# Kernel tuning notes

Hardware: AMD Instinct MI355X
Metric: run time of the kernel (lower is better)

## Reference

```python
import jax, jax.numpy as jnp
import numpy as np

B, S, E = 2, 2048, 1024
H = 16
D = E // H  # head dim

def setup_inputs() -> dict:
    key = jax.random.key(0)
    ks = jax.random.split(key, 9)
    s = 1.0 / np.sqrt(E)
    return {
        "hidden_states": jax.random.normal(ks[0], (B, S, E), dtype=jnp.float32),
        "Wq": jax.random.normal(ks[1], (E, E), dtype=jnp.float32) * s,
        "bq": jnp.zeros((E,), jnp.float32),
        "Wk": jax.random.normal(ks[2], (E, E), dtype=jnp.float32) * s,
        "bk": jnp.zeros((E,), jnp.float32),
        "Wv": jax.random.normal(ks[3], (E, E), dtype=jnp.float32) * s,
        "bv": jnp.zeros((E,), jnp.float32),
        "Wo": jax.random.normal(ks[4], (E, E), dtype=jnp.float32) * s,
        "bo": jnp.zeros((E,), jnp.float32),
    }

def _split_heads(x):
    # [B,S,E] -> [B,H,S,D]
    b, s, _ = x.shape
    return x.reshape(b, s, H, D).transpose(0, 2, 1, 3)

def reference(hidden_states, Wq, bq, Wk, bk, Wv, bv, Wo, bo):
    q = _split_heads(hidden_states @ Wq + bq)  # [B,H,S,D]
    k = _split_heads(hidden_states @ Wk + bk)
    v = _split_heads(hidden_states @ Wv + bv)
    scores = jnp.einsum('bhqd,bhkd->bhqk', q, k) / jnp.sqrt(jnp.float32(D))
    probs = jax.nn.softmax(scores, axis=-1)  # [B,H,S,S]
    ctx = jnp.einsum('bhqk,bhkd->bhqd', probs, v)
    ctx = ctx.transpose(0, 2, 1, 3).reshape(hidden_states.shape[0], -1, E)
    out = ctx @ Wo + bo
    return out, probs
```

## Files before the change

### kernel.cpp

```cpp
#include <hip/hip_runtime.h>
#include <hip/hip_bf16.h>
#include <stdint.h>


typedef __attribute__((ext_vector_type(8))) short bf16x8;
typedef __attribute__((ext_vector_type(4))) short bf16x4v;
typedef __attribute__((ext_vector_type(4))) float f32x4;

#define DEV static __device__ __forceinline__

DEV short f2bs(float f) {
  union { __hip_bfloat16 b; short s; } u;
  u.b = __float2bfloat16(f);
  return u.s;
}
DEV f32x4 mfma16(bf16x8 a, bf16x8 b, f32x4 c) {
  return __builtin_amdgcn_mfma_f32_16x16x32_bf16(a, b, c, 0, 0, 0);
}
DEV float fexp2(float x) { return __builtin_amdgcn_exp2f(x); }
typedef const __attribute__((address_space(1))) void* gas1_t;
typedef __attribute__((address_space(3))) void* las3_t;
DEV void gload_lds16(const void* g, void* l) {
  __builtin_amdgcn_global_load_lds((gas1_t)(uintptr_t)g, (las3_t)(uint32_t)(uintptr_t)l,
                                   16, 0, 0);
}
#define WAIT_VMCNT(N) asm volatile("s_waitcnt vmcnt(" #N ")" ::: "memory")
#define WAIT_LGKM0() asm volatile("s_waitcnt lgkmcnt(0)" ::: "memory")
#define BARRIER() do { __builtin_amdgcn_s_barrier(); __builtin_amdgcn_sched_barrier(0); } while (0)

__global__ void cvt_all_kernel(const float* __restrict__ X,
                               const float* __restrict__ Wq, const float* __restrict__ Wk,
                               const float* __restrict__ Wv, const float* __restrict__ Wo,
                               short* __restrict__ Xb, short* __restrict__ Wt) {
  __shared__ short tile[64][68];
  int bx = blockIdx.x, t = threadIdx.x;
  if (bx < 2048) {
    size_t i = (size_t)bx * 256 + t;
    const float4* X4 = (const float4*)X;
    float4 a = X4[2 * i], c = X4[2 * i + 1];
    bf16x8 o;
    o[0] = f2bs(a.x); o[1] = f2bs(a.y); o[2] = f2bs(a.z); o[3] = f2bs(a.w);
    o[4] = f2bs(c.x); o[5] = f2bs(c.y); o[6] = f2bs(c.z); o[7] = f2bs(c.w);
    *(bf16x8*)(Xb + i * 8) = o;
    return;
  }
  int wb = bx - 2048;
  int mat = wb >> 8, rem = wb & 255;
  const float* W = mat == 0 ? Wq : mat == 1 ? Wk : mat == 2 ? Wv : Wo;
  int kb = (rem >> 4) * 64, nb = (rem & 15) * 64;
#pragma unroll
  for (int it = 0; it < 4; ++it) {
    int idx = it * 256 + t;
    int row = idx >> 4, c4 = (idx & 15) * 4;
    float4 v = *(const float4*)(W + (size_t)(kb + row) * 1024 + nb + c4);
    tile[row][c4 + 0] = f2bs(v.x); tile[row][c4 + 1] = f2bs(v.y);
    tile[row][c4 + 2] = f2bs(v.z); tile[row][c4 + 3] = f2bs(v.w);
  }
  __syncthreads();
#pragma unroll
  for (int it = 0; it < 4; ++it) {
    int idx = it * 256 + t;
    int rn = idx >> 4, c4 = (idx & 15) * 4;
    bf16x4v o;
    o[0] = tile[c4 + 0][rn]; o[1] = tile[c4 + 1][rn];
    o[2] = tile[c4 + 2][rn]; o[3] = tile[c4 + 3][rn];
    *(bf16x4v*)(Wt + (((size_t)mat) << 20) + (size_t)(nb + rn) * 1024 + kb + c4) = o;
  }
}

template <int MODE, int GBX>
__global__ __launch_bounds__(256, 2)
void gemm_bt_kernel(const short* __restrict__ A, const short* __restrict__ Bt,
                    const float* __restrict__ bias0, const float* __restrict__ bias1,
                    const float* __restrict__ bias2,
                    short* __restrict__ o0, short* __restrict__ o1, short* __restrict__ o2,
                    float* __restrict__ fout) {
  __shared__ short As[2][128 * 32];
  __shared__ short Bs[2][128 * 32];
  const int nwg = GBX * gridDim.y;
  const int cpx = nwg >> 3;
  const int bid0 = blockIdx.y * GBX + blockIdx.x;
  const int bid = (bid0 % 8) * cpx + bid0 / 8;
  const int m0 = (bid % GBX) * 128, n0 = (bid / GBX) * 128;
  const int t = threadIdx.x, w = t >> 6, l = t & 63, g = l >> 4, r = l & 15;
  const int wr = (w >> 1) * 64, wc = (w & 1) * 64;
  f32x4 acc[4][4] = {};

#define STAGE_G(k0_, b_)                                                                   \
  do {                                                                                     \
    gload_lds16(A + (size_t)(m0 + (t >> 2)) * 1024 + (k0_) + (t & 3) * 8, As[b_] + w * 512); \
    gload_lds16(A + (size_t)(m0 + 64 + (t >> 2)) * 1024 + (k0_) + (t & 3) * 8,             \
                As[b_] + 2048 + w * 512);                                                  \
    gload_lds16(Bt + (size_t)(n0 + (t >> 2)) * 1024 + (k0_) + (t & 3) * 8, Bs[b_] + w * 512); \
    gload_lds16(Bt + (size_t)(n0 + 64 + (t >> 2)) * 1024 + (k0_) + (t & 3) * 8,            \
                Bs[b_] + 2048 + w * 512);                                                  \
  } while (0)

  STAGE_G(0, 0);
  for (int it = 0; it < 32; ++it) {
    const int cur = it & 1;
    if (it < 31) {
      STAGE_G((it + 1) * 32, cur ^ 1);
      WAIT_VMCNT(4);
    } else {
      WAIT_VMCNT(0);
    }
    BARRIER();
    bf16x8 af[4], bfv[4];
#pragma unroll
    for (int i = 0; i < 4; i++) af[i] = *(const bf16x8*)(As[cur] + (wr + i * 16 + r) * 32 + g * 8);
#pragma unroll
    for (int j = 0; j < 4; j++) bfv[j] = *(const bf16x8*)(Bs[cur] + (wc + j * 16 + r) * 32 + g * 8);
    __builtin_amdgcn_s_setprio(1);
#pragma unroll
    for (int i = 0; i < 4; i++)
#pragma unroll
      for (int j = 0; j < 4; j++) acc[i][j] = mfma16(af[i], bfv[j], acc[i][j]);
    __builtin_amdgcn_s_setprio(0);
    BARRIER();
  }
#undef STAGE_G
  if constexpr (MODE == 0) {
#pragma unroll
    for (int j = 0; j < 4; j++) {
      int ng = n0 + wc + j * 16 + r;
      int mat = ng >> 10, nn = ng & 1023, hh = nn >> 6, dd = nn & 63;
      const float* bp = mat == 0 ? bias0 : (mat == 1 ? bias1 : bias2);
      short* dst = mat == 0 ? o0 : (mat == 1 ? o1 : o2);
      float bv = bp[nn];
      float sc = (mat == 0) ? 0.18033688f : 1.0f;
#pragma unroll
      for (int i = 0; i < 4; i++) {
#pragma unroll
        for (int q = 0; q < 4; q++) {
          int m = m0 + wr + i * 16 + g * 4 + q;
          int bb = m >> 11, ss = m & 2047;
          dst[((size_t)(bb * 16 + hh) * 2048 + ss) * 64 + dd] = f2bs((acc[i][j][q] + bv) * sc);
        }
      }
    }
  } else {
#pragma unroll
    for (int i = 0; i < 4; i++)
#pragma unroll
      for (int q = 0; q < 4; q++) {
        int m = m0 + wr + i * 16 + g * 4 + q;
#pragma unroll
        for (int j = 0; j < 4; j++) {
          int ng = n0 + wc + j * 16 + r;
          fout[(size_t)m * 1024 + ng] = acc[i][j][q] + bias0[ng];
        }
      }
  }
}

__global__ __launch_bounds__(256, 2)
void attn_kernel(const short* __restrict__ Qm, const short* __restrict__ Km,
                 const short* __restrict__ Vm, float* __restrict__ probs,
                 short* __restrict__ ctx) {
  __shared__ short Ks[2][128 * 64];
  __shared__ short Vt[64 * 136];
  __shared__ short Ps[4][16 * 136];
  __shared__ float rls[128];
  const int f = blockIdx.x;
  const int wgid = (f & 7) * 64 + (f >> 3);
  const int bh = wgid >> 4, q0 = (wgid & 15) * 128;
  const int bb = bh >> 4, hh = bh & 15;
  const short* Qp = Qm + (size_t)bh * 2048 * 64;
  const short* Kp = Km + (size_t)bh * 2048 * 64;
  const short* Vp = Vm + (size_t)bh * 2048 * 64;
  float* Pp = probs + (size_t)bh * 2048 * 2048;
  const int t = threadIdx.x, w = t >> 6, l = t & 63, g = l >> 4, r = l & 15;
  const int lr = l >> 3, lc = l & 7;
  const int swz = lc ^ lr;

#define STAGE_K(kt_, buf_)                                                            \
  do {                                                                                \
    const short* src_ = Kp + (size_t)((kt_) * 128) * 64;                              \
    _Pragma("unroll") for (int it_ = 0; it_ < 4; ++it_)                               \
        gload_lds16(src_ + (size_t)(it_ * 32 + w * 8 + lr) * 64 + swz * 8,            \
                    Ks[buf_] + (it_ * 32 + w * 8) * 64);                              \
  } while (0)

#pragma unroll
  for (int it = 0; it < 2; ++it) {
    gload_lds16(Qp + (size_t)(q0 + it * 32 + w * 8 + lr) * 64 + swz * 8,
                Ks[0] + (it * 32 + w * 8) * 64);
    gload_lds16(Qp + (size_t)(q0 + 64 + it * 32 + w * 8 + lr) * 64 + swz * 8,
                Ks[1] + (it * 32 + w * 8) * 64);
  }
  __syncthreads();
  bf16x8 qf0[2], qf1[2];
#pragma unroll
  for (int df = 0; df < 2; df++) {
    qf0[df] = *(const bf16x8*)(Ks[0] + (w * 16 + r) * 64 + ((df * 4 + g) ^ (r & 7)) * 8);
    qf1[df] = *(const bf16x8*)(Ks[1] + (w * 16 + r) * 64 + ((df * 4 + g) ^ (r & 7)) * 8);
  }
  WAIT_LGKM0();
  BARRIER();

  float lrow0 = 0.f;
  STAGE_K(0, 0);
  for (int kt = 0; kt < 16; ++kt) {
    const int cur = kt & 1;
    if (kt < 15) {
      STAGE_K(kt + 1, cur ^ 1);
      WAIT_VMCNT(4);
    } else {
      WAIT_VMCNT(0);
    }
    BARRIER();
    f32x4 st[8] = {};
    __builtin_amdgcn_s_setprio(1);
#pragma unroll
    for (int df = 0; df < 2; ++df) {
      bf16x8 kf[8];
#pragma unroll
      for (int ni = 0; ni < 8; ni++)
        kf[ni] = *(const bf16x8*)(Ks[cur] + (ni * 16 + r) * 64 + ((df * 4 + g) ^ (r & 7)) * 8);
#pragma unroll
      for (int ni = 0; ni < 8; ni++) st[ni] = mfma16(kf[ni], qf0[df], st[ni]);
    }
    __builtin_amdgcn_s_setprio(0);
    float ssum = 0.f;
#pragma unroll
    for (int ni = 0; ni < 8; ni++)
#pragma unroll
      for (int q4 = 0; q4 < 4; q4++) ssum += fexp2(st[ni][q4]);
    ssum += __shfl_xor(ssum, 16);
    ssum += __shfl_xor(ssum, 32);
    lrow0 += ssum;
    BARRIER();
  }
  const float rinv0 = 1.0f / lrow0;
  if (g == 0) rls[w * 16 + r] = rinv0;

  const int kp = (t >> 3) * 2, d0v = (t & 7) * 8, lcv = t & 7, kunit = t >> 5;

#define B_TILE_BODY(stv_, qrow_, rinv_)                                                \
  do {                                                                                 \
                              \
    _Pragma("unroll") for (int ni = 0; ni < 8; ni++) {                                 \
      bf16x4v pk;                                                                      \
      _Pragma("unroll") for (int q4 = 0; q4 < 4; q4++) {                               \
        float pe = fexp2((stv_)[ni][q4]);                                              \
        (stv_)[ni][q4] = pe;                                                           \
        pk[q4] = f2bs(pe);                                                             \
      }                                                                                \
      *(bf16x4v*)(&Ps[w][r * 136 + ni * 16 + g * 4]) = pk;                             \
    }                                                                                  \
                               \
    _Pragma("unroll") for (int e = 0; e < 8; e++) {                                    \
      unsigned int p0_ = (unsigned int)(unsigned short)v0[e] |                         \
                         ((unsigned int)(unsigned short)v1[e] << 16);                  \
      unsigned int p1_ = (unsigned int)(unsigned short)v2[e] |                         \
                         ((unsigned int)(unsigned short)v3[e] << 16);                  \
      *(unsigned int*)(Vt + (d0v + e) * 136 + ((kunit ^ lcv) << 3) + (kp & 7)) = p0_;  \
      *(unsigned int*)(Vt + (d0v + e) * 136 + ((8 + (kunit ^ lcv)) << 3) + (kp & 7)) = p1_; \
    }                                                                                  \
    WAIT_LGKM0();                                                                      \
    BARRIER();                                                                         \
              \
    _Pragma("unroll") for (int ni = 0; ni < 8; ni++) {                                 \
      f32x4 pr;                                                                        \
      _Pragma("unroll") for (int q4 = 0; q4 < 4; q4++) pr[q4] = (stv_)[ni][q4] * (rinv_); \
      *(f32x4*)(Pp + (size_t)((qrow_) + w * 16 + r) * 2048 + kt * 128 + ni * 16 + g * 4) = pr; \
    }                                                                                  \
                             \
    __builtin_amdgcn_s_setprio(1);                                                     \
    _Pragma("unroll") for (int kf4 = 0; kf4 < 4; ++kf4) {                              \
      bf16x8 pa, vb[4];                                                                \
      pa = *(const bf16x8*)(&Ps[w][r * 136 + kf4 * 32 + g * 8]);                       \
      _Pragma("unroll") for (int nj = 0; nj < 4; nj++) {                               \
        int u_ = kf4 * 4 + g, x_ = nj * 2 + (r >> 3);                                  \
        int su_ = (u_ & 8) | ((u_ & 7) ^ x_);                                          \
        vb[nj] = *(const bf16x8*)(Vt + (nj * 16 + r) * 136 + (su_ << 3));              \
      }                                                                                \
      _Pragma("unroll") for (int nj = 0; nj < 4; nj++)                                 \
          cacc[nj] = mfma16(pa, vb[nj], cacc[nj]);                                     \
    }                                                                                  \
    __builtin_amdgcn_s_setprio(0);                                                     \
  } while (0)

  f32x4 cacc[4] = {};
  float lrow1 = 0.f;
  STAGE_K(0, 0);
  for (int kt = 0; kt < 16; ++kt) {
    const int cur = kt & 1;
    bf16x8 v0 = *(const bf16x8*)(Vp + (size_t)(kt * 128 + kp) * 64 + d0v);
    bf16x8 v1 = *(const bf16x8*)(Vp + (size_t)(kt * 128 + kp + 1) * 64 + d0v);
    bf16x8 v2 = *(const bf16x8*)(Vp + (size_t)(kt * 128 + 64 + kp) * 64 + d0v);
    bf16x8 v3 = *(const bf16x8*)(Vp + (size_t)(kt * 128 + 64 + kp + 1) * 64 + d0v);
    if (kt < 15) STAGE_K(kt + 1, cur ^ 1);
    if (kt == 0) { WAIT_VMCNT(8); }
    else if (kt < 15) { WAIT_VMCNT(16); }
    else { WAIT_VMCNT(12); }
    BARRIER();
    f32x4 st0[8] = {}, st1[8] = {};
    __builtin_amdgcn_s_setprio(1);
#pragma unroll
    for (int df = 0; df < 2; ++df) {
      bf16x8 kf[8];
#pragma unroll
      for (int ni = 0; ni < 8; ni++)
        kf[ni] = *(const bf16x8*)(Ks[cur] + (ni * 16 + r) * 64 + ((df * 4 + g) ^ (r & 7)) * 8);
#pragma unroll
      for (int ni = 0; ni < 8; ni++) {
        st0[ni] = mfma16(kf[ni], qf0[df], st0[ni]);
        st1[ni] = mfma16(kf[ni], qf1[df], st1[ni]);
      }
    }
    __builtin_amdgcn_s_setprio(0);
    {
      float ssum = 0.f;
#pragma unroll
      for (int ni = 0; ni < 8; ni++)
#pragma unroll
        for (int q4 = 0; q4 < 4; q4++) ssum += fexp2(st1[ni][q4]);
      ssum += __shfl_xor(ssum, 16);
      ssum += __shfl_xor(ssum, 32);
      lrow1 += ssum;
    }
    B_TILE_BODY(st0, q0, rinv0);
  }
#pragma unroll
  for (int nj = 0; nj < 4; nj++)
#pragma unroll
    for (int q4 = 0; q4 < 4; q4++) {
      int qt = w * 16 + g * 4 + q4;
      float val = cacc[nj][q4] * rls[qt];
      ctx[((size_t)(bb * 2048 + q0 + qt)) * 1024 + hh * 64 + nj * 16 + r] = f2bs(val);
    }

  const float rinv1 = 1.0f / lrow1;
  if (g == 0) rls[64 + w * 16 + r] = rinv1;
#pragma unroll
  for (int nj = 0; nj < 4; nj++) cacc[nj] = (f32x4){0.f, 0.f, 0.f, 0.f};
  STAGE_K(0, 0);
  for (int kt = 0; kt < 16; ++kt) {
    const int cur = kt & 1;
    bf16x8 v0 = *(const bf16x8*)(Vp + (size_t)(kt * 128 + kp) * 64 + d0v);
    bf16x8 v1 = *(const bf16x8*)(Vp + (size_t)(kt * 128 + kp + 1) * 64 + d0v);
    bf16x8 v2 = *(const bf16x8*)(Vp + (size_t)(kt * 128 + 64 + kp) * 64 + d0v);
    bf16x8 v3 = *(const bf16x8*)(Vp + (size_t)(kt * 128 + 64 + kp + 1) * 64 + d0v);
    if (kt < 15) STAGE_K(kt + 1, cur ^ 1);
    if (kt == 0) { WAIT_VMCNT(8); }
    else if (kt < 15) { WAIT_VMCNT(16); }
    else { WAIT_VMCNT(12); }
    BARRIER();
    f32x4 st[8] = {};
    __builtin_amdgcn_s_setprio(1);
#pragma unroll
    for (int df = 0; df < 2; ++df) {
      bf16x8 kf[8];
#pragma unroll
      for (int ni = 0; ni < 8; ni++)
        kf[ni] = *(const bf16x8*)(Ks[cur] + (ni * 16 + r) * 64 + ((df * 4 + g) ^ (r & 7)) * 8);
#pragma unroll
      for (int ni = 0; ni < 8; ni++) st[ni] = mfma16(kf[ni], qf1[df], st[ni]);
    }
    __builtin_amdgcn_s_setprio(0);
    B_TILE_BODY(st, q0 + 64, rinv1);
  }
#pragma unroll
  for (int nj = 0; nj < 4; nj++)
#pragma unroll
    for (int q4 = 0; q4 < 4; q4++) {
      int qt = w * 16 + g * 4 + q4;
      float val = cacc[nj][q4] * rls[64 + qt];
      ctx[((size_t)(bb * 2048 + q0 + 64 + qt)) * 1024 + hh * 64 + nj * 16 + r] = f2bs(val);
    }
#undef B_TILE_BODY
#undef STAGE_K
}

extern "C" void kernel_launch(void* const* d_in, const int* in_sizes, int n_in,
                              void* d_out, int out_size, void* d_ws, size_t ws_size,
                              hipStream_t stream) {
  (void)in_sizes; (void)n_in; (void)out_size; (void)ws_size;
  const float* X  = (const float*)d_in[0];
  const float* Wq = (const float*)d_in[1];
  const float* bq = (const float*)d_in[2];
  const float* Wk = (const float*)d_in[3];
  const float* bk = (const float*)d_in[4];
  const float* Wv = (const float*)d_in[5];
  const float* bv = (const float*)d_in[6];
  const float* Wo = (const float*)d_in[7];
  const float* bo = (const float*)d_in[8];
  float* out = (float*)d_out;
  float* probs = out + (size_t)2 * 2048 * 1024;

  short* Xb = (short*)d_ws;
  short* Wt = Xb + (size_t)4194304;
  short* Qb = Wt + (size_t)4194304;
  short* Kb = Qb + (size_t)4194304;
  short* Vb = Kb + (size_t)4194304;
  short* Cx = Vb + (size_t)4194304;

  cvt_all_kernel<<<3072, 256, 0, stream>>>(X, Wq, Wk, Wv, Wo, Xb, Wt);
  gemm_bt_kernel<0, 32><<<dim3(32, 24), 256, 0, stream>>>(Xb, Wt, bq, bk, bv,
                                                          Qb, Kb, Vb, nullptr);
  attn_kernel<<<512, 256, 0, stream>>>(Qb, Kb, Vb, probs, Cx);
  gemm_bt_kernel<1, 32><<<dim3(32, 8), 256, 0, stream>>>(Cx, Wt + (size_t)3 * 1048576, bo,
                                                         nullptr, nullptr, nullptr, nullptr,
                                                         nullptr, out);
}
```

Baseline: 222.6 us.

## Software-pipeline attention tiles so QK MFMA overlaps previous tile's PV and prob stores

Restructures the per-tile attention loop into a two-stage software pipeline with ping-pong score registers. Each iteration computes QK^T for tile kt and then finishes tile kt-1 (normalized prob stores and the PV MFMAs) before exponentiating and staging the current tile's P and V into LDS. This is meant to hide the LDS barrier and exp latency behind MFMA work. In exchange it holds two score buffers live, which raises register pressure, and it needs more intricate vmcnt waits that must stay correct.

```diff
diff --git a/kernel.cpp b/kernel.cpp
--- a/kernel.cpp
+++ b/kernel.cpp
@@ -237,36 +237,19 @@
 
   const int kp = (t >> 3) * 2, d0v = (t & 7) * 8, lcv = t & 7, kunit = t >> 5;
 
-#define B_TILE_BODY(stv_, qrow_, rinv_)                                                \
+#define V_LOADS(kt_)                                                                   \
+  v0 = *(const bf16x8*)(Vp + (size_t)((kt_) * 128 + kp) * 64 + d0v);                   \
+  v1 = *(const bf16x8*)(Vp + (size_t)((kt_) * 128 + kp + 1) * 64 + d0v);               \
+  v2 = *(const bf16x8*)(Vp + (size_t)((kt_) * 128 + 64 + kp) * 64 + d0v);              \
+  v3 = *(const bf16x8*)(Vp + (size_t)((kt_) * 128 + 64 + kp + 1) * 64 + d0v)
+
+#define FIN_T(stP_, qrow_, rinv_, ktF_)                                                \
   do {                                                                                 \
-                              \
-    _Pragma("unroll") for (int ni = 0; ni < 8; ni++) {                                 \
-      bf16x4v pk;                                                                      \
-      _Pragma("unroll") for (int q4 = 0; q4 < 4; q4++) {                               \
-        float pe = fexp2((stv_)[ni][q4]);                                              \
-        (stv_)[ni][q4] = pe;                                                           \
-        pk[q4] = f2bs(pe);                                                             \
-      }                                                                                \
-      *(bf16x4v*)(&Ps[w][r * 136 + ni * 16 + g * 4]) = pk;                             \
-    }                                                                                  \
-                               \
-    _Pragma("unroll") for (int e = 0; e < 8; e++) {                                    \
-      unsigned int p0_ = (unsigned int)(unsigned short)v0[e] |                         \
-                         ((unsigned int)(unsigned short)v1[e] << 16);                  \
-      unsigned int p1_ = (unsigned int)(unsigned short)v2[e] |                         \
-                         ((unsigned int)(unsigned short)v3[e] << 16);                  \
-      *(unsigned int*)(Vt + (d0v + e) * 136 + ((kunit ^ lcv) << 3) + (kp & 7)) = p0_;  \
-      *(unsigned int*)(Vt + (d0v + e) * 136 + ((8 + (kunit ^ lcv)) << 3) + (kp & 7)) = p1_; \
-    }                                                                                  \
-    WAIT_LGKM0();                                                                      \
-    BARRIER();                                                                         \
-              \
     _Pragma("unroll") for (int ni = 0; ni < 8; ni++) {                                 \
       f32x4 pr;                                                                        \
-      _Pragma("unroll") for (int q4 = 0; q4 < 4; q4++) pr[q4] = (stv_)[ni][q4] * (rinv_); \
-      *(f32x4*)(Pp + (size_t)((qrow_) + w * 16 + r) * 2048 + kt * 128 + ni * 16 + g * 4) = pr; \
-    }                                                                                  \
-                             \
+      _Pragma("unroll") for (int q4 = 0; q4 < 4; q4++) pr[q4] = (stP_)[ni][q4] * (rinv_); \
+      *(f32x4*)(Pp + (size_t)((qrow_) + w * 16 + r) * 2048 + (ktF_) * 128 + ni * 16 + g * 4) = pr; \
+    }                                                                                  \
     __builtin_amdgcn_s_setprio(1);                                                     \
     _Pragma("unroll") for (int kf4 = 0; kf4 < 4; ++kf4) {                              \
       bf16x8 pa, vb[4];                                                                \
@@ -282,46 +265,87 @@
     __builtin_amdgcn_s_setprio(0);                                                     \
   } while (0)
 
+#define B_ITER(kt_, stC_, stP_, HAS_FIN, FIRST, SECOND, LAST, T1, qf_, qrow_, rinv_)   \
+  do {                                                                                 \
+    const int cur_ = (kt_) & 1;                                                        \
+    bf16x4v pk[8];                                                                     \
+    V_LOADS(kt_);                                                                      \
+    if (!(LAST)) STAGE_K((kt_) + 1, cur_ ^ 1);                                         \
+    if ((FIRST) || (SECOND)) { WAIT_VMCNT(8); }                                        \
+    else if (LAST) { WAIT_VMCNT(12); }                                                 \
+    else { WAIT_VMCNT(16); }                                                           \
+    BARRIER();                                                                         \
+    __builtin_amdgcn_s_setprio(1);                                                     \
+    _Pragma("unroll") for (int df = 0; df < 2; ++df) {                                 \
+      bf16x8 kf[8];                                                                    \
+      _Pragma("unroll") for (int ni = 0; ni < 8; ni++)                                 \
+          kf[ni] = *(const bf16x8*)(Ks[cur_] + (ni * 16 + r) * 64 +                    \
+                                    ((df * 4 + g) ^ (r & 7)) * 8);                     \
+      _Pragma("unroll") for (int ni = 0; ni < 8; ni++) {                               \
+        (stC_)[ni] = mfma16(kf[ni], qf_[df], (stC_)[ni]);                              \
+        if (T1) st1[ni] = mfma16(kf[ni], qf1[df], st1[ni]);                            \
+      }                                                                                \
+    }                                                                                  \
+    __builtin_amdgcn_s_setprio(0);                                                     \
+    if (HAS_FIN) FIN_T(stP_, qrow_, rinv_, (kt_)-1);                                   \
+    _Pragma("unroll") for (int ni = 0; ni < 8; ni++) {                                 \
+      _Pragma("unroll") for (int q4 = 0; q4 < 4; q4++) {                               \
+        float pe = fexp2((stC_)[ni][q4]);                                              \
+        (stC_)[ni][q4] = pe;                                                           \
+        pk[ni][q4] = f2bs(pe);                                                         \
+      }                                                                                \
+    }                                                                                  \
+    if (T1) {                                                                          \
+      float ssum = 0.f;                                                                \
+      _Pragma("unroll") for (int ni = 0; ni < 8; ni++)                                 \
+          _Pragma("unroll") for (int q4 = 0; q4 < 4; q4++) ssum += fexp2(st1[ni][q4]); \
+      ssum += __shfl_xor(ssum, 16);                                                    \
+      ssum += __shfl_xor(ssum, 32);                                                    \
+      lrow1 += ssum;                                                                   \
+    }                                                                                  \
+    BARRIER();                                                                         \
+    if (FIRST) { WAIT_VMCNT(4); }                                                      \
+    else if (LAST) { WAIT_VMCNT(8); }                                                  \
+    else { WAIT_VMCNT(12); }                                                           \
+    _Pragma("unroll") for (int e = 0; e < 8; e++) {                                    \
+      unsigned int p0_ = (unsigned int)(unsigned short)v0[e] |                         \
+                         ((unsigned int)(unsigned short)v1[e] << 16);                  \
+      unsigned int p1_ = (unsigned int)(unsigned short)v2[e] |                         \
+                         ((unsigned int)(unsigned short)v3[e] << 16);                  \
+      *(unsigned int*)(Vt + (d0v + e) * 136 + ((kunit ^ lcv) << 3) + (kp & 7)) = p0_;  \
+      *(unsigned int*)(Vt + (d0v + e) * 136 + ((8 + (kunit ^ lcv)) << 3) + (kp & 7)) = p1_; \
+    }                                                                                  \
+    _Pragma("unroll") for (int ni = 0; ni < 8; ni++)                                   \
+        *(bf16x4v*)(&Ps[w][r * 136 + ni * 16 + g * 4]) = pk[ni];                       \
+    WAIT_LGKM0();                                                                      \
+  } while (0)
+
   f32x4 cacc[4] = {};
   float lrow1 = 0.f;
-  STAGE_K(0, 0);
-  for (int kt = 0; kt < 16; ++kt) {
-    const int cur = kt & 1;
-    bf16x8 v0 = *(const bf16x8*)(Vp + (size_t)(kt * 128 + kp) * 64 + d0v);
-    bf16x8 v1 = *(const bf16x8*)(Vp + (size_t)(kt * 128 + kp + 1) * 64 + d0v);
-    bf16x8 v2 = *(const bf16x8*)(Vp + (size_t)(kt * 128 + 64 + kp) * 64 + d0v);
-    bf16x8 v3 = *(const bf16x8*)(Vp + (size_t)(kt * 128 + 64 + kp + 1) * 64 + d0v);
-    if (kt < 15) STAGE_K(kt + 1, cur ^ 1);
-    if (kt == 0) { WAIT_VMCNT(8); }
-    else if (kt < 15) { WAIT_VMCNT(16); }
-    else { WAIT_VMCNT(12); }
-    BARRIER();
-    f32x4 st0[8] = {}, st1[8] = {};
-    __builtin_amdgcn_s_setprio(1);
-#pragma unroll
-    for (int df = 0; df < 2; ++df) {
-      bf16x8 kf[8];
-#pragma unroll
-      for (int ni = 0; ni < 8; ni++)
-        kf[ni] = *(const bf16x8*)(Ks[cur] + (ni * 16 + r) * 64 + ((df * 4 + g) ^ (r & 7)) * 8);
-#pragma unroll
-      for (int ni = 0; ni < 8; ni++) {
-        st0[ni] = mfma16(kf[ni], qf0[df], st0[ni]);
-        st1[ni] = mfma16(kf[ni], qf1[df], st1[ni]);
+  {
+    bf16x8 v0, v1, v2, v3;
+    f32x4 stA[8], stB[8], st1z[8];
+    f32x4* st1 = st1z;
+    STAGE_K(0, 0);
+    for (int i2 = 0; i2 < 8; ++i2) {
+#pragma unroll
+      for (int ni = 0; ni < 8; ni++) stA[ni] = (f32x4){0.f, 0.f, 0.f, 0.f};
+#pragma unroll
+      for (int ni = 0; ni < 8; ni++) st1[ni] = (f32x4){0.f, 0.f, 0.f, 0.f};
+      if (i2 == 0) {
+        B_ITER(0, stA, stB, false, true, false, false, true, qf0, q0, rinv0);
+      } else {
+        B_ITER(2 * i2, stA, stB, true, false, false, false, true, qf0, q0, rinv0);
       }
-    }
-    __builtin_amdgcn_s_setprio(0);
-    {
-      float ssum = 0.f;
-#pragma unroll
-      for (int ni = 0; ni < 8; ni++)
-#pragma unroll
-        for (int q4 = 0; q4 < 4; q4++) ssum += fexp2(st1[ni][q4]);
-      ssum += __shfl_xor(ssum, 16);
-      ssum += __shfl_xor(ssum, 32);
-      lrow1 += ssum;
-    }
-    B_TILE_BODY(st0, q0, rinv0);
+#pragma unroll
+      for (int ni = 0; ni < 8; ni++) stB[ni] = (f32x4){0.f, 0.f, 0.f, 0.f};
+#pragma unroll
+      for (int ni = 0; ni < 8; ni++) st1[ni] = (f32x4){0.f, 0.f, 0.f, 0.f};
+      B_ITER(2 * i2 + 1, stB, stA, true, false, (i2 == 0), (i2 == 7), true,
+             qf0, q0, rinv0);
+    }
+    BARRIER();
+    FIN_T(stB, q0, rinv0, 15);
   }
 #pragma unroll
   for (int nj = 0; nj < 4; nj++)
@@ -336,31 +360,27 @@
   if (g == 0) rls[64 + w * 16 + r] = rinv1;
 #pragma unroll
   for (int nj = 0; nj < 4; nj++) cacc[nj] = (f32x4){0.f, 0.f, 0.f, 0.f};
-  STAGE_K(0, 0);
-  for (int kt = 0; kt < 16; ++kt) {
-    const int cur = kt & 1;
-    bf16x8 v0 = *(const bf16x8*)(Vp + (size_t)(kt * 128 + kp) * 64 + d0v);
-    bf16x8 v1 = *(const bf16x8*)(Vp + (size_t)(kt * 128 + kp + 1) * 64 + d0v);
-    bf16x8 v2 = *(const bf16x8*)(Vp + (size_t)(kt * 128 + 64 + kp) * 64 + d0v);
-    bf16x8 v3 = *(const bf16x8*)(Vp + (size_t)(kt * 128 + 64 + kp + 1) * 64 + d0v);
-    if (kt < 15) STAGE_K(kt + 1, cur ^ 1);
-    if (kt == 0) { WAIT_VMCNT(8); }
-    else if (kt < 15) { WAIT_VMCNT(16); }
-    else { WAIT_VMCNT(12); }
-    BARRIER();
-    f32x4 st[8] = {};
-    __builtin_amdgcn_s_setprio(1);
-#pragma unroll
-    for (int df = 0; df < 2; ++df) {
-      bf16x8 kf[8];
-#pragma unroll
-      for (int ni = 0; ni < 8; ni++)
-        kf[ni] = *(const bf16x8*)(Ks[cur] + (ni * 16 + r) * 64 + ((df * 4 + g) ^ (r & 7)) * 8);
-#pragma unroll
-      for (int ni = 0; ni < 8; ni++) st[ni] = mfma16(kf[ni], qf1[df], st[ni]);
-    }
-    __builtin_amdgcn_s_setprio(0);
-    B_TILE_BODY(st, q0 + 64, rinv1);
+  {
+    bf16x8 v0, v1, v2, v3;
+    f32x4 stA[8], stB[8];
+    f32x4* st1 = nullptr;
+    STAGE_K(0, 0);
+    for (int i2 = 0; i2 < 8; ++i2) {
+#pragma unroll
+      for (int ni = 0; ni < 8; ni++) stA[ni] = (f32x4){0.f, 0.f, 0.f, 0.f};
+      if (i2 == 0) {
+        B_ITER(0, stA, stB, false, true, false, false, false, qf1, q0 + 64, rinv1);
+      } else {
+        B_ITER(2 * i2, stA, stB, true, false, false, false, false, qf1, q0 + 64, rinv1);
+      }
+#pragma unroll
+      for (int ni = 0; ni < 8; ni++) stB[ni] = (f32x4){0.f, 0.f, 0.f, 0.f};
+      B_ITER(2 * i2 + 1, stB, stA, true, false, (i2 == 0), (i2 == 7), false,
+             qf1, q0 + 64, rinv1);
+    }
+    BARRIER();
+    FIN_T(stB, q0 + 64, rinv1, 15);
+    (void)st1;
   }
 #pragma unroll
   for (int nj = 0; nj < 4; nj++)
@@ -370,7 +390,9 @@
       float val = cacc[nj][q4] * rls[64 + qt];
       ctx[((size_t)(bb * 2048 + q0 + 64 + qt)) * 1024 + hh * 64 + nj * 16 + r] = f2bs(val);
     }
-#undef B_TILE_BODY
+#undef B_ITER
+#undef FIN_T
+#undef V_LOADS
 #undef STAGE_K
 }
 
```

Result: no change. 224.9 us (+1.0%).

## Double GEMM K-tile to 64 with XOR-swizzled LDS and narrower output-projection tiles

Applied to the files above, without the earlier changes.

The GEMM kernel now stages 64-wide K slices instead of 32, halving the main-loop iterations and barriers, and applies an XOR swizzle on the LDS layout so the wider rows avoid bank conflicts. The output-projection instance switches to 128x64 tiles with a doubled grid and a higher occupancy hint, giving more workgroups for the 256-tile problem. The cost is larger LDS use per block and more in-flight loads, which could limit occupancy for the QKV projection.

```diff
diff --git a/kernel.cpp b/kernel.cpp
--- a/kernel.cpp
+++ b/kernel.cpp
@@ -69,53 +69,67 @@
 }
 
 template <int MODE, int GBX>
-__global__ __launch_bounds__(256, 2)
+__global__ __launch_bounds__(256, MODE == 0 ? 2 : 3)
 void gemm_bt_kernel(const short* __restrict__ A, const short* __restrict__ Bt,
                     const float* __restrict__ bias0, const float* __restrict__ bias1,
                     const float* __restrict__ bias2,
                     short* __restrict__ o0, short* __restrict__ o1, short* __restrict__ o2,
                     float* __restrict__ fout) {
-  __shared__ short As[2][128 * 32];
-  __shared__ short Bs[2][128 * 32];
+  constexpr int BN = (MODE == 0) ? 128 : 64;
+  constexpr int NBLINES = BN / 32;
+  __shared__ short As[2][128 * 64];
+  __shared__ short Bs[2][BN * 64];
   const int nwg = GBX * gridDim.y;
   const int cpx = nwg >> 3;
   const int bid0 = blockIdx.y * GBX + blockIdx.x;
   const int bid = (bid0 % 8) * cpx + bid0 / 8;
-  const int m0 = (bid % GBX) * 128, n0 = (bid / GBX) * 128;
+  const int m0 = (bid % GBX) * 128, n0 = (bid / GBX) * BN;
   const int t = threadIdx.x, w = t >> 6, l = t & 63, g = l >> 4, r = l & 15;
-  const int wr = (w >> 1) * 64, wc = (w & 1) * 64;
-  f32x4 acc[4][4] = {};
-
-#define STAGE_G(k0_, b_)                                                                   \
-  do {                                                                                     \
-    gload_lds16(A + (size_t)(m0 + (t >> 2)) * 1024 + (k0_) + (t & 3) * 8, As[b_] + w * 512); \
-    gload_lds16(A + (size_t)(m0 + 64 + (t >> 2)) * 1024 + (k0_) + (t & 3) * 8,             \
-                As[b_] + 2048 + w * 512);                                                  \
-    gload_lds16(Bt + (size_t)(n0 + (t >> 2)) * 1024 + (k0_) + (t & 3) * 8, Bs[b_] + w * 512); \
-    gload_lds16(Bt + (size_t)(n0 + 64 + (t >> 2)) * 1024 + (k0_) + (t & 3) * 8,            \
-                Bs[b_] + 2048 + w * 512);                                                  \
+  const int lr = l >> 3, lc = l & 7;
+  const int swz = lc ^ lr;
+  const int wr = (w >> 1) * 64, wc = (w & 1) * (BN / 2);
+  f32x4 acc[4][BN / 32] = {};
+
+#define STAGE_G(k0_, b_)                                                                \
+  do {                                                                                  \
+    _Pragma("unroll") for (int it_ = 0; it_ < 4; ++it_)                                 \
+        gload_lds16(A + (size_t)(m0 + it_ * 32 + w * 8 + lr) * 1024 + (k0_) + swz * 8,  \
+                    As[b_] + (it_ * 32 + w * 8) * 64);                                  \
+    _Pragma("unroll") for (int it_ = 0; it_ < NBLINES; ++it_)                           \
+        gload_lds16(Bt + (size_t)(n0 + it_ * 32 + w * 8 + lr) * 1024 + (k0_) + swz * 8, \
+                    Bs[b_] + (it_ * 32 + w * 8) * 64);                                  \
   } while (0)
 
   STAGE_G(0, 0);
-  for (int it = 0; it < 32; ++it) {
+  for (int it = 0; it < 16; ++it) {
     const int cur = it & 1;
-    if (it < 31) {
-      STAGE_G((it + 1) * 32, cur ^ 1);
-      WAIT_VMCNT(4);
+    if (it < 15) {
+      STAGE_G((it + 1) * 64, cur ^ 1);
+      if constexpr (MODE == 0) { WAIT_VMCNT(8); } else { WAIT_VMCNT(6); }
     } else {
       WAIT_VMCNT(0);
     }
     BARRIER();
-    bf16x8 af[4], bfv[4];
-#pragma unroll
-    for (int i = 0; i < 4; i++) af[i] = *(const bf16x8*)(As[cur] + (wr + i * 16 + r) * 32 + g * 8);
-#pragma unroll
-    for (int j = 0; j < 4; j++) bfv[j] = *(const bf16x8*)(Bs[cur] + (wc + j * 16 + r) * 32 + g * 8);
+    bf16x8 af[2][4], bfv[2][BN / 32];
+#pragma unroll
+    for (int df = 0; df < 2; df++) {
+#pragma unroll
+      for (int i = 0; i < 4; i++)
+        af[df][i] = *(const bf16x8*)(As[cur] + (wr + i * 16 + r) * 64 +
+                                     ((df * 4 + g) ^ (r & 7)) * 8);
+#pragma unroll
+      for (int j = 0; j < BN / 32; j++)
+        bfv[df][j] = *(const bf16x8*)(Bs[cur] + (wc + j * 16 + r) * 64 +
+                                      ((df * 4 + g) ^ (r & 7)) * 8);
+    }
     __builtin_amdgcn_s_setprio(1);
 #pragma unroll
-    for (int i = 0; i < 4; i++)
-#pragma unroll
-      for (int j = 0; j < 4; j++) acc[i][j] = mfma16(af[i], bfv[j], acc[i][j]);
+    for (int df = 0; df < 2; df++)
+#pragma unroll
+      for (int i = 0; i < 4; i++)
+#pragma unroll
+        for (int j = 0; j < BN / 32; j++)
+          acc[i][j] = mfma16(af[df][i], bfv[df][j], acc[i][j]);
     __builtin_amdgcn_s_setprio(0);
     BARRIER();
   }
@@ -146,7 +160,7 @@
       for (int q = 0; q < 4; q++) {
         int m = m0 + wr + i * 16 + g * 4 + q;
 #pragma unroll
-        for (int j = 0; j < 4; j++) {
+        for (int j = 0; j < 2; j++) {
           int ng = n0 + wc + j * 16 + r;
           fout[(size_t)m * 1024 + ng] = acc[i][j][q] + bias0[ng];
         }
@@ -401,7 +415,7 @@
   gemm_bt_kernel<0, 32><<<dim3(32, 24), 256, 0, stream>>>(Xb, Wt, bq, bk, bv,
                                                           Qb, Kb, Vb, nullptr);
   attn_kernel<<<512, 256, 0, stream>>>(Qb, Kb, Vb, probs, Cx);
-  gemm_bt_kernel<1, 32><<<dim3(32, 8), 256, 0, stream>>>(Cx, Wt + (size_t)3 * 1048576, bo,
-                                                         nullptr, nullptr, nullptr, nullptr,
-                                                         nullptr, out);
-}
+  gemm_bt_kernel<1, 32><<<dim3(32, 16), 256, 0, stream>>>(Cx, Wt + (size_t)3 * 1048576, bo,
+                                                          nullptr, nullptr, nullptr, nullptr,
+                                                          nullptr, out);
+}
```

After: 212.8 us, median of 4. 4.4% less time.
